# Kernel optimization log

Measured on AMD Instinct MI355X. Metric: run time of the kernel, lower is better.

Reference implementation:

```python
import jax, jax.numpy as jnp
import numpy as np

NC = 6          # num_classes
RM = 16         # reg_max
TOPK = 10       # tal_topk
IMG = 640.0
STRIDES = (8, 16, 32)
BS = 32
NGT = 20        # GT boxes per image (uniform -> static max_boxes)


def _iou(b1, b2, ciou, eps=1e-7):
    x1 = jnp.maximum(b1[..., 0], b2[..., 0]); y1 = jnp.maximum(b1[..., 1], b2[..., 1])
    x2 = jnp.minimum(b1[..., 2], b2[..., 2]); y2 = jnp.minimum(b1[..., 3], b2[..., 3])
    inter = jnp.maximum(x2 - x1, 0.0) * jnp.maximum(y2 - y1, 0.0)
    w1 = jnp.maximum(b1[..., 2] - b1[..., 0], eps); h1 = jnp.maximum(b1[..., 3] - b1[..., 1], eps)
    w2 = jnp.maximum(b2[..., 2] - b2[..., 0], eps); h2 = jnp.maximum(b2[..., 3] - b2[..., 1], eps)
    union = w1 * h1 + w2 * h2 - inter + eps
    iou = inter / union
    if not ciou:
        return iou
    cw = jnp.maximum(b1[..., 2], b2[..., 2]) - jnp.minimum(b1[..., 0], b2[..., 0])
    ch = jnp.maximum(b1[..., 3], b2[..., 3]) - jnp.minimum(b1[..., 1], b2[..., 1])
    c2 = cw ** 2 + ch ** 2 + eps
    rho2 = ((b1[..., 0] + b1[..., 2] - b2[..., 0] - b2[..., 2]) ** 2
            + (b1[..., 1] + b1[..., 3] - b2[..., 1] - b2[..., 3]) ** 2) / 4.0
    v = (4.0 / (np.pi ** 2)) * (jnp.arctan(w2 / h2) - jnp.arctan(w1 / h1)) ** 2
    alpha = jax.lax.stop_gradient(v / (v - iou + (1.0 + eps)))
    return iou - (rho2 / c2 + v * alpha)


def _forward(p0, p1, p2, targets):
    bs = p0.shape[0]
    regs, clss, ancs, strs = [], [], [], []
    for p, s in zip((p0, p1, p2), STRIDES):
        b, c, h, w = p.shape
        p = jnp.transpose(p, (0, 2, 3, 1)).reshape(b, h * w, c)
        regs.append(p[..., :4 * RM].reshape(b, h * w, 4, RM))
        clss.append(p[..., 4 * RM:])
        gy, gx = jnp.meshgrid(jnp.arange(h), jnp.arange(w), indexing='ij')
        ancs.append(((jnp.stack([gx, gy], -1).astype(jnp.float32) + 0.5) * s).reshape(-1, 2))
        strs.append(jnp.full((h * w, 1), float(s), jnp.float32))
    pred_reg = jnp.concatenate(regs, 1)      # [bs, A, 4, RM]
    pred_cls = jnp.concatenate(clss, 1)      # [bs, A, NC]
    anchors = jnp.concatenate(ancs, 0)       # [A, 2] pixel coords
    stride_a = jnp.concatenate(strs, 0)      # [A, 1]
    A = anchors.shape[0]

    proj = jnp.arange(RM, dtype=jnp.float32)
    pd_dist = jnp.sum(jax.nn.softmax(pred_reg, -1) * proj, -1)       # [bs, A, 4]
    anc_b = jnp.broadcast_to(anchors[None], (bs, A, 2))
    pd_boxes = jnp.concatenate([anc_b - pd_dist[..., :2] * stride_a,
                                anc_b + pd_dist[..., 2:] * stride_a], -1)

    # GT parse: exactly NGT rows per image, grouped by image index (static reshape)
    G = targets.shape[0] // bs
    t = targets.reshape(bs, G, 6)
    gt_labels = t[..., 1]
    xywh = t[..., 2:6] * IMG
    gt_boxes = jnp.concatenate([xywh[..., :2] - xywh[..., 2:] / 2,
                                xywh[..., :2] + xywh[..., 2:] / 2], -1)  # [bs, G, 4]
    mask_gt = jnp.ones((bs, G, 1), jnp.float32)

    # ---- task-aligned assignment (on detached preds) ----
    pscore = jax.nn.sigmoid(jax.lax.stop_gradient(pred_cls))
    pbox_d = jax.lax.stop_gradient(pd_boxes)
    ious = _iou(gt_boxes[:, :, None, :], pbox_d[:, None, :, :], False)   # [bs, G, A]
    labels_i = gt_labels.astype(jnp.int32)
    scores = jnp.einsum('bac,bgc->bga', pscore, jax.nn.one_hot(labels_i, NC, dtype=pscore.dtype))
    align = (scores ** 0.5) * (ious ** 6.0)
    lt = anc_b[:, None, :, :] - gt_boxes[:, :, None, :2]
    rb = gt_boxes[:, :, None, 2:] - anc_b[:, None, :, :]
    in_gts = jnp.min(jnp.concatenate([lt, rb], -1), -1) > 1e-9
    align = align * in_gts * mask_gt
    _, tk_idx = jax.lax.top_k(align, TOPK)
    bi = jnp.arange(bs)[:, None, None]; gi = jnp.arange(G)[None, :, None]
    mask_pos = jnp.zeros((bs, G, A), bool).at[bi, gi, tk_idx].set(True)
    mask_pos = mask_pos & (align > 0)
    multi = jnp.sum(mask_pos, 1) > 1                                   # [bs, A]
    full = jnp.moveaxis(jax.nn.one_hot(jnp.argmax(align, 1), G), -1, 1) > 0.5
    mask_pos = jnp.where(multi[:, None, :], full, mask_pos)

    fg = jnp.any(mask_pos, 1)                                          # [bs, A]
    gt_idx = jnp.argmax(mask_pos, 1)                                   # [bs, A] (first True)
    tb = jnp.take_along_axis(gt_boxes, jnp.broadcast_to(gt_idx[..., None], (bs, A, 4)), axis=1)
    target_boxes = jnp.where(fg[..., None], tb, 0.0)
    t_lab = jnp.take_along_axis(labels_i, gt_idx, axis=1)
    iou_fg = jnp.maximum(jax.lax.stop_gradient(_iou(pd_boxes, target_boxes, False)), 0.0)
    norm_align = align / (jnp.max(align, -1, keepdims=True) + 1e-9)
    norm_g = jnp.take_along_axis(norm_align, gt_idx[:, None, :], axis=1)[:, 0, :]
    sval = jnp.where(fg, norm_g * iou_fg, 0.0)
    target_scores = sval[..., None] * jax.nn.one_hot(t_lab, NC, dtype=jnp.float32)

    # cls: BCE with logits, sum / num_anchors
    x = pred_cls
    bce = jnp.maximum(x, 0.0) - x * target_scores + jnp.log1p(jnp.exp(-jnp.abs(x)))
    loss_cls = jnp.sum(bce) / float(A)

    fgf = fg.astype(jnp.float32)
    num_pos = jnp.maximum(jnp.sum(fgf), 1.0)

    # bbox: 1 - CIoU over positives
    ciou = _iou(pd_boxes, target_boxes, True)
    loss_bbox = jnp.sum((1.0 - ciou) * fgf) / num_pos

    # DFL
    ltrb = jnp.concatenate([(anc_b - target_boxes[..., :2]) / stride_a,
                            (target_boxes[..., 2:] - anc_b) / stride_a], -1)
    ltrb = jnp.clip(ltrb, 0.0, RM - 1.01)
    tl = ltrb.astype(jnp.int32)
    wl = (tl + 1).astype(jnp.float32) - ltrb
    wr = ltrb - tl.astype(jnp.float32)
    logZ = jax.nn.logsumexp(pred_reg, -1)                              # [bs, A, 4]
    ce_l = logZ - jnp.take_along_axis(pred_reg, tl[..., None], -1)[..., 0]
    ce_r = logZ - jnp.take_along_axis(pred_reg, (tl + 1)[..., None], -1)[..., 0]
    loss_dfl = jnp.sum(jnp.sum(ce_l * wl + ce_r * wr, -1) * fgf) / num_pos

    l_cls = loss_cls * 1.0
    l_bbox = loss_bbox * 7.5
    l_dfl = loss_dfl * 1.5
    return jnp.stack([l_cls + l_bbox + l_dfl, l_cls, l_bbox, jnp.asarray(0.0, jnp.float32), l_dfl])


def setup_inputs() -> dict:
    key = jax.random.key(0)
    k0, k1, k2, k3, k4, k5 = jax.random.split(key, 6)
    C = 4 * RM + NC
    p0 = jax.random.normal(k0, (BS, C, 80, 80), jnp.float32)
    p1 = jax.random.normal(k1, (BS, C, 40, 40), jnp.float32)
    p2 = jax.random.normal(k2, (BS, C, 20, 20), jnp.float32)
    bidx = jnp.repeat(jnp.arange(BS), NGT).astype(jnp.float32)
    lab = jax.random.randint(k3, (BS * NGT,), 0, NC).astype(jnp.float32)
    cxcy = jax.random.uniform(k4, (BS * NGT, 2), minval=0.2, maxval=0.8)
    wh = jax.random.uniform(k5, (BS * NGT, 2), minval=0.05, maxval=0.3)
    targets = jnp.concatenate([bidx[:, None], lab[:, None], cxcy, wh], 1)
    return {"p0": p0, "p1": p1, "p2": p2, "targets": targets}


def reference(p0, p1, p2, targets):
    return _forward(p0, p1, p2, targets)
```

## Files before the change

### kernel.cpp

```cpp
#include <hip/hip_runtime.h>
#include <math.h>

#define NC 6
#define RM 16
#define TOPK 10
#define BSZ 32
#define G 20
#define A_TOT 8400
#define NBA (BSZ * A_TOT)
#define NBLK_LOSS ((NBA + 255) / 256)
#define NBLK_PREP ((NBA / 4 + 255) / 256)
#define MAXCAND 1024

#define COMP(v4, j) ((j) == 0 ? (v4).x : (j) == 1 ? (v4).y : (j) == 2 ? (v4).z : (v4).w)

__device__ __forceinline__ void anchor_decode(int a, int& lvl, int& ai, int& w, int& hw, float& s) {
    if (a < 6400)      { lvl = 0; ai = a;        w = 80; hw = 6400; s = 8.f; }
    else if (a < 8000) { lvl = 1; ai = a - 6400; w = 40; hw = 1600; s = 16.f; }
    else               { lvl = 2; ai = a - 8000; w = 20; hw = 400;  s = 32.f; }
}

__device__ __forceinline__ float align_from(const float* __restrict__ trow, float logit,
                                            float4 box, float ax, float ay) {
    float cx = trow[2] * 640.f, cy = trow[3] * 640.f;
    float hwd = trow[4] * 320.f, hh = trow[5] * 320.f;
    float gx1 = cx - hwd, gy1 = cy - hh, gx2 = cx + hwd, gy2 = cy + hh;
    float mn = fminf(fminf(ax - gx1, ay - gy1), fminf(gx2 - ax, gy2 - ay));
    if (mn <= 1e-9f) return 0.f;
    const float eps = 1e-7f;
    float x1 = fmaxf(gx1, box.x), y1 = fmaxf(gy1, box.y);
    float x2 = fminf(gx2, box.z), y2 = fminf(gy2, box.w);
    float inter = fmaxf(x2 - x1, 0.f) * fmaxf(y2 - y1, 0.f);
    float gw = fmaxf(gx2 - gx1, eps), gh = fmaxf(gy2 - gy1, eps);
    float w2 = fmaxf(box.z - box.x, eps), h2 = fmaxf(box.w - box.y, eps);
    float uni = gw * gh + w2 * h2 - inter + eps;
    float iou = inter / uni;
    float sc = 1.f / (1.f + __expf(-logit));
    float i2 = iou * iou;
    return sqrtf(sc) * (i2 * i2 * i2);
}

__global__ __launch_bounds__(256) void k_prep(
        const float* __restrict__ p0, const float* __restrict__ p1, const float* __restrict__ p2,
        float* __restrict__ pd_boxes, float* __restrict__ logZ,
        unsigned int* __restrict__ mask, float* __restrict__ partial_prep) {
    int tid = blockIdx.x * 256 + threadIdx.x;
    int idx4 = tid * 4;
    float bce = 0.f;
    if (idx4 < NBA) {
        int b = idx4 / A_TOT, a4 = idx4 % A_TOT;
        int lvl, ai, w, hw; float s;
        anchor_decode(a4, lvl, ai, w, hw, s);
        const float* p = (lvl == 0) ? p0 : ((lvl == 1) ? p1 : p2);
        const float* base = p + (size_t)b * 70 * hw + ai;
        float ay = ((float)(ai / w) + 0.5f) * s;
        float ax0 = ((float)(ai % w) + 0.5f) * s;

        float4 dist0, dist1, dist2, dist3, lz0, lz1, lz2, lz3;
        auto do_side = [&](int sd, float4& dist, float4& lz) {
            float4 v[RM];
            float4 m = make_float4(-1e30f, -1e30f, -1e30f, -1e30f);
            #pragma unroll
            for (int k = 0; k < RM; ++k) {
                v[k] = *(const float4*)(base + (size_t)(sd * RM + k) * hw);
                m.x = fmaxf(m.x, v[k].x); m.y = fmaxf(m.y, v[k].y);
                m.z = fmaxf(m.z, v[k].z); m.w = fmaxf(m.w, v[k].w);
            }
            float4 se = make_float4(0, 0, 0, 0), sk = make_float4(0, 0, 0, 0);
            #pragma unroll
            for (int k = 0; k < RM; ++k) {
                float fk = (float)k;
                float ex = __expf(v[k].x - m.x); se.x += ex; sk.x += ex * fk;
                float ey = __expf(v[k].y - m.y); se.y += ey; sk.y += ey * fk;
                float ez = __expf(v[k].z - m.z); se.z += ez; sk.z += ez * fk;
                float ew = __expf(v[k].w - m.w); se.w += ew; sk.w += ew * fk;
            }
            dist = make_float4(sk.x / se.x, sk.y / se.y, sk.z / se.z, sk.w / se.w);
            lz = make_float4(m.x + __logf(se.x), m.y + __logf(se.y),
                             m.z + __logf(se.z), m.w + __logf(se.w));
        };
        do_side(0, dist0, lz0);
        do_side(1, dist1, lz1);
        do_side(2, dist2, lz2);
        do_side(3, dist3, lz3);

        #pragma unroll
        for (int j = 0; j < 4; ++j) {
            float axj = ax0 + (float)j * s;
            float4 bx = make_float4(axj - COMP(dist0, j) * s, ay - COMP(dist1, j) * s,
                                    axj + COMP(dist2, j) * s, ay + COMP(dist3, j) * s);
            ((float4*)pd_boxes)[idx4 + j] = bx;
            ((float4*)logZ)[idx4 + j] =
                make_float4(COMP(lz0, j), COMP(lz1, j), COMP(lz2, j), COMP(lz3, j));
        }
        #pragma unroll
        for (int c = 0; c < NC; ++c) {
            float4 x = *(const float4*)(base + (size_t)(64 + c) * hw);
            bce += fmaxf(x.x, 0.f) + __logf(1.f + __expf(-fabsf(x.x)));
            bce += fmaxf(x.y, 0.f) + __logf(1.f + __expf(-fabsf(x.y)));
            bce += fmaxf(x.z, 0.f) + __logf(1.f + __expf(-fabsf(x.z)));
            bce += fmaxf(x.w, 0.f) + __logf(1.f + __expf(-fabsf(x.w)));
        }
        ((uint4*)mask)[tid] = make_uint4(0, 0, 0, 0);
    }
    __shared__ float part[4];
    int lane = threadIdx.x & 63, wv = threadIdx.x >> 6;
    #pragma unroll
    for (int off = 32; off > 0; off >>= 1) bce += __shfl_down(bce, off);
    if (lane == 0) part[wv] = bce;
    __syncthreads();
    if (threadIdx.x == 0)
        partial_prep[blockIdx.x] = part[0] + part[1] + part[2] + part[3];
}

__device__ __forceinline__ bool cand_better(float av, int ai_, float bv, int bi_) {
    if (av > bv) return true;
    if (av < bv) return false;
    if (ai_ < 0) return false;
    if (bi_ < 0) return true;
    return ai_ < bi_;
}

__global__ __launch_bounds__(256) void k_align(
        const float* __restrict__ targets,
        const float* __restrict__ pd_boxes,
        const float* __restrict__ p0, const float* __restrict__ p1, const float* __restrict__ p2,
        float* __restrict__ amax, unsigned int* __restrict__ mask) {
    __shared__ float cval[MAXCAND];
    __shared__ int   cidx[MAXCAND];
    __shared__ int   cnt_s;
    __shared__ float rv[4];
    __shared__ int   ri[4];
    __shared__ int   win_i_s;

    int bg = blockIdx.x;
    int b = bg / G;
    int g = bg % G;
    const float* t = targets + (size_t)bg * 6;
    int lab = (int)t[1];
    const float* cb0 = p0 + (size_t)b * 70 * 6400 + (size_t)(64 + lab) * 6400;
    const float* cb1 = p1 + (size_t)b * 70 * 1600 + (size_t)(64 + lab) * 1600;
    const float* cb2 = p2 + (size_t)b * 70 * 400  + (size_t)(64 + lab) * 400;
    const float4* pb = (const float4*)pd_boxes + (size_t)b * A_TOT;

    if (threadIdx.x == 0) cnt_s = 0;
    __syncthreads();

    for (int a = threadIdx.x; a < A_TOT; a += 256) {
        int lvl, ai, w_, hwc; float s;
        anchor_decode(a, lvl, ai, w_, hwc, s);
        float ax = ((ai % w_) + 0.5f) * s, ay = ((ai / w_) + 0.5f) * s;
        float logit = (lvl == 0) ? cb0[ai] : ((lvl == 1) ? cb1[ai] : cb2[ai]);
        float al = align_from(t, logit, pb[a], ax, ay);
        if (al > 0.f) {
            int p = atomicAdd(&cnt_s, 1);
            if (p < MAXCAND) { cval[p] = al; cidx[p] = a; }
        }
    }
    __syncthreads();
    int cnt = min(cnt_s, MAXCAND);

    float mv[MAXCAND / 256];
    int   mi[MAXCAND / 256];
    #pragma unroll
    for (int r = 0; r < MAXCAND / 256; ++r) {
        int p = threadIdx.x + r * 256;
        mv[r] = (p < cnt) ? cval[p] : -1.f;
        mi[r] = (p < cnt) ? cidx[p] : -1;
    }

    int lane = threadIdx.x & 63, wv = threadIdx.x >> 6;
    for (int it = 0; it < TOPK; ++it) {
        float v = -1.f; int vi = -1;
        #pragma unroll
        for (int r = 0; r < MAXCAND / 256; ++r)
            if (cand_better(mv[r], mi[r], v, vi)) { v = mv[r]; vi = mi[r]; }
        #pragma unroll
        for (int off = 32; off > 0; off >>= 1) {
            float ov = __shfl_down(v, off);
            int   oi = __shfl_down(vi, off);
            if (cand_better(ov, oi, v, vi)) { v = ov; vi = oi; }
        }
        if (lane == 0) { rv[wv] = v; ri[wv] = vi; }
        __syncthreads();
        if (threadIdx.x == 0) {
            float v0 = rv[0]; int i0 = ri[0];
            for (int i = 1; i < 4; ++i)
                if (cand_better(rv[i], ri[i], v0, i0)) { v0 = rv[i]; i0 = ri[i]; }
            if (it == 0) amax[bg] = fmaxf(v0, 0.f);
            if (i0 >= 0 && v0 > 0.f) atomicOr(&mask[(size_t)b * A_TOT + i0], 1u << g);
            win_i_s = i0;
        }
        __syncthreads();
        int wi = win_i_s;
        if (wi < 0) break;
        #pragma unroll
        for (int r = 0; r < MAXCAND / 256; ++r)
            if (mi[r] == wi) { mv[r] = -1.f; mi[r] = -1; }
    }
}

__global__ __launch_bounds__(256) void k_loss(
        const float* __restrict__ targets,
        const float* __restrict__ pd_boxes, const float* __restrict__ logZ,
        const float* __restrict__ amax, const unsigned int* __restrict__ mask,
        const float* __restrict__ p0, const float* __restrict__ p1, const float* __restrict__ p2,
        float* __restrict__ partial) {
    int idx = blockIdx.x * 256 + threadIdx.x;
    float bce_s = 0.f, bbox_s = 0.f, dfl_s = 0.f, fg_s = 0.f;
    if (idx < NBA) {
        unsigned int m = mask[idx];
        if (m != 0u) {
            int b = idx / A_TOT, a = idx % A_TOT;
            int lvl, ai, w_, hw; float s;
            anchor_decode(a, lvl, ai, w_, hw, s);
            const float* p = (lvl == 0) ? p0 : ((lvl == 1) ? p1 : p2);
            const float* base = p + (size_t)b * 70 * hw + ai;
            float ax = ((ai % w_) + 0.5f) * s, ay = ((ai / w_) + 0.5f) * s;
            float4 box = ((const float4*)pd_boxes)[idx];
            int gidx;
            if (__popc(m) > 1) {
                float best = -1.f; gidx = 0;
                for (int g = 0; g < G; ++g) {
                    const float* tg = targets + ((size_t)b * G + g) * 6;
                    int labg = (int)tg[1];
                    float al = align_from(tg, base[(size_t)(64 + labg) * hw], box, ax, ay);
                    if (al > best) { best = al; gidx = g; }
                }
            } else {
                gidx = __ffs(m) - 1;
            }
            const float* t = targets + ((size_t)b * G + gidx) * 6;
            int lab = (int)t[1];
            float logit = base[(size_t)(64 + lab) * hw];
            float al = align_from(t, logit, box, ax, ay);
            float cx = t[2] * 640.f, cy = t[3] * 640.f;
            float hwd = t[4] * 320.f, hh = t[5] * 320.f;
            float tbx1 = cx - hwd, tby1 = cy - hh, tbx2 = cx + hwd, tby2 = cy + hh;
            const float eps = 1e-7f;
            float x1 = fmaxf(box.x, tbx1), y1 = fmaxf(box.y, tby1);
            float x2 = fminf(box.z, tbx2), y2 = fminf(box.w, tby2);
            float inter = fmaxf(x2 - x1, 0.f) * fmaxf(y2 - y1, 0.f);
            float w1 = fmaxf(box.z - box.x, eps), h1 = fmaxf(box.w - box.y, eps);
            float w2 = fmaxf(tbx2 - tbx1, eps), h2 = fmaxf(tby2 - tby1, eps);
            float uni = w1 * h1 + w2 * h2 - inter + eps;
            float iou = inter / uni;
            float iou_fg = fmaxf(iou, 0.f);
            float sval = (al / (amax[b * G + gidx] + 1e-9f)) * iou_fg;
            bce_s = -logit * sval;
            fg_s = 1.f;
            float cw = fmaxf(box.z, tbx2) - fminf(box.x, tbx1);
            float ch = fmaxf(box.w, tby2) - fminf(box.y, tby1);
            float c2 = cw * cw + ch * ch + eps;
            float dx = box.x + box.z - tbx1 - tbx2;
            float dy = box.y + box.w - tby1 - tby2;
            float rho2 = (dx * dx + dy * dy) * 0.25f;
            float dv = atanf(w2 / h2) - atanf(w1 / h1);
            float v = 0.40528473f * dv * dv;
            float alpha = v / (v - iou + (1.f + eps));
            float ciou = iou - (rho2 / c2 + v * alpha);
            bbox_s = 1.f - ciou;
            float4 lzv = ((const float4*)logZ)[idx];
            float lz[4] = {lzv.x, lzv.y, lzv.z, lzv.w};
            float lt[4] = {(ax - tbx1) / s, (ay - tby1) / s, (tbx2 - ax) / s, (tby2 - ay) / s};
            #pragma unroll
            for (int sd = 0; sd < 4; ++sd) {
                float d = fminf(fmaxf(lt[sd], 0.f), (float)RM - 1.01f);
                int tl = (int)d;
                float wl = (float)(tl + 1) - d;
                float wr = d - (float)tl;
                float xl = base[(size_t)(sd * RM + tl) * hw];
                float xr = base[(size_t)(sd * RM + tl + 1) * hw];
                dfl_s += (lz[sd] - xl) * wl + (lz[sd] - xr) * wr;
            }
        }
    }
    __shared__ float part[4][4];
    int lane = threadIdx.x & 63, wv = threadIdx.x >> 6;
    #pragma unroll
    for (int off = 32; off > 0; off >>= 1) {
        bce_s  += __shfl_down(bce_s,  off);
        bbox_s += __shfl_down(bbox_s, off);
        dfl_s  += __shfl_down(dfl_s,  off);
        fg_s   += __shfl_down(fg_s,   off);
    }
    if (lane == 0) {
        part[wv][0] = bce_s; part[wv][1] = bbox_s;
        part[wv][2] = dfl_s; part[wv][3] = fg_s;
    }
    __syncthreads();
    if (threadIdx.x == 0) {
        float s0 = 0.f, s1 = 0.f, s2 = 0.f, s3 = 0.f;
        for (int i = 0; i < 4; ++i) {
            s0 += part[i][0]; s1 += part[i][1]; s2 += part[i][2]; s3 += part[i][3];
        }
        ((float4*)partial)[blockIdx.x] = make_float4(s0, s1, s2, s3);
    }
}

__global__ __launch_bounds__(256) void k_final(const float* __restrict__ partial,
                                               const float* __restrict__ partial_prep,
                                               float* __restrict__ out) {
    double s0 = 0., s1 = 0., s2 = 0., s3 = 0.;
    for (int i = threadIdx.x; i < NBLK_LOSS; i += 256) {
        float4 p = ((const float4*)partial)[i];
        s0 += p.x; s1 += p.y; s2 += p.z; s3 += p.w;
    }
    for (int i = threadIdx.x; i < NBLK_PREP; i += 256)
        s0 += partial_prep[i];
    #pragma unroll
    for (int off = 32; off > 0; off >>= 1) {
        s0 += __shfl_down(s0, off);
        s1 += __shfl_down(s1, off);
        s2 += __shfl_down(s2, off);
        s3 += __shfl_down(s3, off);
    }
    __shared__ double part[4][4];
    int lane = threadIdx.x & 63, wv = threadIdx.x >> 6;
    if (lane == 0) { part[wv][0] = s0; part[wv][1] = s1; part[wv][2] = s2; part[wv][3] = s3; }
    __syncthreads();
    if (threadIdx.x == 0) {
        double bce = 0., bbox = 0., dfl = 0., fgc = 0.;
        for (int i = 0; i < 4; ++i) {
            bce += part[i][0]; bbox += part[i][1]; dfl += part[i][2]; fgc += part[i][3];
        }
        double l_cls = bce / (double)A_TOT;
        double np_ = fmax(fgc, 1.0);
        double l_bbox = 7.5 * bbox / np_;
        double l_dfl = 1.5 * dfl / np_;
        out[0] = (float)(l_cls + l_bbox + l_dfl);
        out[1] = (float)l_cls;
        out[2] = (float)l_bbox;
        out[3] = 0.f;
        out[4] = (float)l_dfl;
    }
}

extern "C" void kernel_launch(void* const* d_in, const int* in_sizes, int n_in,
                              void* d_out, int out_size, void* d_ws, size_t ws_size,
                              hipStream_t stream) {
    const float* p0 = (const float*)d_in[0];
    const float* p1 = (const float*)d_in[1];
    const float* p2 = (const float*)d_in[2];
    const float* targets = (const float*)d_in[3];
    float* out = (float*)d_out;

    char* ws = (char*)d_ws;
    size_t off = 0;
    float* pd_boxes = (float*)(ws + off); off += (size_t)NBA * 4 * sizeof(float);
    float* logZ     = (float*)(ws + off); off += (size_t)NBA * 4 * sizeof(float);
    float* amax     = (float*)(ws + off); off += (size_t)BSZ * G * sizeof(float);
    unsigned int* mask = (unsigned int*)(ws + off); off += (size_t)NBA * sizeof(unsigned int);
    float* partial  = (float*)(ws + off); off += (size_t)NBLK_LOSS * 4 * sizeof(float);
    float* partial_prep = (float*)(ws + off); off += (size_t)NBLK_PREP * sizeof(float);

    k_prep<<<NBLK_PREP, 256, 0, stream>>>(p0, p1, p2, pd_boxes, logZ, mask, partial_prep);
    k_align<<<BSZ * G, 256, 0, stream>>>(targets, pd_boxes, p0, p1, p2, amax, mask);
    k_loss<<<NBLK_LOSS, 256, 0, stream>>>(targets, pd_boxes, logZ, amax, mask,
                                          p0, p1, p2, partial);
    k_final<<<1, 256, 0, stream>>>(partial, partial_prep, out);
}
```

Before: 157.8 us.

## Split prep kernel work across four threads per anchor quad via shared memory

The prep kernel now assigns one thread per box side (four threads per group of four anchors) instead of one thread doing all four sides. Each thread computes the softmax/logsumexp for its side, writes it to shared memory, then after a barrier assembles one anchor's box and logZ. The BCE work over the six class channels is also split across the four threads. This raises parallelism and cuts per-thread register pressure and serial work, at the cost of a shared-memory exchange, a block barrier and a larger grid.

Result: faster. 148.6 us (-5.8%).

```diff
diff --git a/kernel.cpp b/kernel.cpp
--- a/kernel.cpp
+++ b/kernel.cpp
@@ -9,10 +9,8 @@
 #define A_TOT 8400
 #define NBA (BSZ * A_TOT)
 #define NBLK_LOSS ((NBA + 255) / 256)
-#define NBLK_PREP ((NBA / 4 + 255) / 256)
+#define NBLK_PREP (NBA / 256)
 #define MAXCAND 1024
-
-#define COMP(v4, j) ((j) == 0 ? (v4).x : (j) == 1 ? (v4).y : (j) == 2 ? (v4).z : (v4).w)
 
 __device__ __forceinline__ void anchor_decode(int a, int& lvl, int& ai, int& w, int& hw, float& s) {
     if (a < 6400)      { lvl = 0; ai = a;        w = 80; hw = 6400; s = 8.f; }
@@ -44,65 +42,69 @@
         const float* __restrict__ p0, const float* __restrict__ p1, const float* __restrict__ p2,
         float* __restrict__ pd_boxes, float* __restrict__ logZ,
         unsigned int* __restrict__ mask, float* __restrict__ partial_prep) {
+    __shared__ float sdist[256 * 4];
+    __shared__ float slz[256 * 4];
     int tid = blockIdx.x * 256 + threadIdx.x;
-    int idx4 = tid * 4;
+    int q = tid >> 2;
+    int sd = tid & 3;
+    int idx4 = q * 4;
+    int b = idx4 / A_TOT, a4 = idx4 % A_TOT;
+    int lvl, ai, w, hw; float s;
+    anchor_decode(a4, lvl, ai, w, hw, s);
+    const float* p = (lvl == 0) ? p0 : ((lvl == 1) ? p1 : p2);
+    const float* base = p + (size_t)b * 70 * hw + ai;
+
+    float4 v[RM];
+    float4 m = make_float4(-1e30f, -1e30f, -1e30f, -1e30f);
+    #pragma unroll
+    for (int k = 0; k < RM; ++k) {
+        v[k] = *(const float4*)(base + (size_t)(sd * RM + k) * hw);
+        m.x = fmaxf(m.x, v[k].x); m.y = fmaxf(m.y, v[k].y);
+        m.z = fmaxf(m.z, v[k].z); m.w = fmaxf(m.w, v[k].w);
+    }
+    float4 se = make_float4(0, 0, 0, 0), sk = make_float4(0, 0, 0, 0);
+    #pragma unroll
+    for (int k = 0; k < RM; ++k) {
+        float fk = (float)k;
+        float ex = __expf(v[k].x - m.x); se.x += ex; sk.x += ex * fk;
+        float ey = __expf(v[k].y - m.y); se.y += ey; sk.y += ey * fk;
+        float ez = __expf(v[k].z - m.z); se.z += ez; sk.z += ez * fk;
+        float ew = __expf(v[k].w - m.w); se.w += ew; sk.w += ew * fk;
+    }
+    ((float4*)sdist)[threadIdx.x] =
+        make_float4(sk.x / se.x, sk.y / se.y, sk.z / se.z, sk.w / se.w);
+    ((float4*)slz)[threadIdx.x] =
+        make_float4(m.x + __logf(se.x), m.y + __logf(se.y),
+                    m.z + __logf(se.z), m.w + __logf(se.w));
+
     float bce = 0.f;
-    if (idx4 < NBA) {
-        int b = idx4 / A_TOT, a4 = idx4 % A_TOT;
-        int lvl, ai, w, hw; float s;
-        anchor_decode(a4, lvl, ai, w, hw, s);
-        const float* p = (lvl == 0) ? p0 : ((lvl == 1) ? p1 : p2);
-        const float* base = p + (size_t)b * 70 * hw + ai;
-        float ay = ((float)(ai / w) + 0.5f) * s;
-        float ax0 = ((float)(ai % w) + 0.5f) * s;
-
-        float4 dist0, dist1, dist2, dist3, lz0, lz1, lz2, lz3;
-        auto do_side = [&](int sd, float4& dist, float4& lz) {
-            float4 v[RM];
-            float4 m = make_float4(-1e30f, -1e30f, -1e30f, -1e30f);
-            #pragma unroll
-            for (int k = 0; k < RM; ++k) {
-                v[k] = *(const float4*)(base + (size_t)(sd * RM + k) * hw);
-                m.x = fmaxf(m.x, v[k].x); m.y = fmaxf(m.y, v[k].y);
-                m.z = fmaxf(m.z, v[k].z); m.w = fmaxf(m.w, v[k].w);
-            }
-            float4 se = make_float4(0, 0, 0, 0), sk = make_float4(0, 0, 0, 0);
-            #pragma unroll
-            for (int k = 0; k < RM; ++k) {
-                float fk = (float)k;
-                float ex = __expf(v[k].x - m.x); se.x += ex; sk.x += ex * fk;
-                float ey = __expf(v[k].y - m.y); se.y += ey; sk.y += ey * fk;
-                float ez = __expf(v[k].z - m.z); se.z += ez; sk.z += ez * fk;
-                float ew = __expf(v[k].w - m.w); se.w += ew; sk.w += ew * fk;
-            }
-            dist = make_float4(sk.x / se.x, sk.y / se.y, sk.z / se.z, sk.w / se.w);
-            lz = make_float4(m.x + __logf(se.x), m.y + __logf(se.y),
-                             m.z + __logf(se.z), m.w + __logf(se.w));
-        };
-        do_side(0, dist0, lz0);
-        do_side(1, dist1, lz1);
-        do_side(2, dist2, lz2);
-        do_side(3, dist3, lz3);
-
-        #pragma unroll
-        for (int j = 0; j < 4; ++j) {
-            float axj = ax0 + (float)j * s;
-            float4 bx = make_float4(axj - COMP(dist0, j) * s, ay - COMP(dist1, j) * s,
-                                    axj + COMP(dist2, j) * s, ay + COMP(dist3, j) * s);
-            ((float4*)pd_boxes)[idx4 + j] = bx;
-            ((float4*)logZ)[idx4 + j] =
-                make_float4(COMP(lz0, j), COMP(lz1, j), COMP(lz2, j), COMP(lz3, j));
-        }
-        #pragma unroll
-        for (int c = 0; c < NC; ++c) {
-            float4 x = *(const float4*)(base + (size_t)(64 + c) * hw);
-            bce += fmaxf(x.x, 0.f) + __logf(1.f + __expf(-fabsf(x.x)));
-            bce += fmaxf(x.y, 0.f) + __logf(1.f + __expf(-fabsf(x.y)));
-            bce += fmaxf(x.z, 0.f) + __logf(1.f + __expf(-fabsf(x.z)));
-            bce += fmaxf(x.w, 0.f) + __logf(1.f + __expf(-fabsf(x.w)));
-        }
-        ((uint4*)mask)[tid] = make_uint4(0, 0, 0, 0);
-    }
+    {
+        float4 x = *(const float4*)(base + (size_t)(64 + sd) * hw);
+        bce += fmaxf(x.x, 0.f) + __logf(1.f + __expf(-fabsf(x.x)));
+        bce += fmaxf(x.y, 0.f) + __logf(1.f + __expf(-fabsf(x.y)));
+        bce += fmaxf(x.z, 0.f) + __logf(1.f + __expf(-fabsf(x.z)));
+        bce += fmaxf(x.w, 0.f) + __logf(1.f + __expf(-fabsf(x.w)));
+        if (sd < 2) {
+            float4 y = *(const float4*)(base + (size_t)(68 + sd) * hw);
+            bce += fmaxf(y.x, 0.f) + __logf(1.f + __expf(-fabsf(y.x)));
+            bce += fmaxf(y.y, 0.f) + __logf(1.f + __expf(-fabsf(y.y)));
+            bce += fmaxf(y.z, 0.f) + __logf(1.f + __expf(-fabsf(y.z)));
+            bce += fmaxf(y.w, 0.f) + __logf(1.f + __expf(-fabsf(y.w)));
+        }
+    }
+    mask[tid] = 0u;
+    __syncthreads();
+
+    int gb = (threadIdx.x & ~3) * 4;
+    float d0 = sdist[gb + sd], d1 = sdist[gb + 4 + sd];
+    float d2 = sdist[gb + 8 + sd], d3 = sdist[gb + 12 + sd];
+    float z0 = slz[gb + sd], z1 = slz[gb + 4 + sd];
+    float z2 = slz[gb + 8 + sd], z3 = slz[gb + 12 + sd];
+    float ax = ((float)(ai % w + sd) + 0.5f) * s;
+    float ay = ((float)(ai / w) + 0.5f) * s;
+    ((float4*)pd_boxes)[tid] = make_float4(ax - d0 * s, ay - d1 * s, ax + d2 * s, ay + d3 * s);
+    ((float4*)logZ)[tid] = make_float4(z0, z1, z2, z3);
+
     __shared__ float part[4];
     int lane = threadIdx.x & 63, wv = threadIdx.x >> 6;
     #pragma unroll
```
